# Performance work log

Measured on AMD Instinct MI355X. Metric: run time of the kernel, lower is better.

## Reference

```python
import jax, jax.numpy as jnp
import numpy as np

B, Cin, Cout, H, W = 4, 256, 256, 64, 64
DG, KH, KW = 2, 3, 3        # deformable_groups=2, kernel 3x3
K = KH * KW
CG = Cin // DG


def setup_inputs() -> dict:
    key = jax.random.key(0)
    ks = jax.random.split(key, 4)
    x = jax.random.normal(ks[0], (B, Cin, H, W), jnp.float32)
    # offset/mask-predicting 3x3 conv: 3*DG*K = 54 output channels
    # (small weights so sampled offsets stay in a realistic +-few-pixel range)
    w_off = jax.random.normal(ks[1], (3 * DG * K, Cin, KH, KW), jnp.float32) * 0.01
    b_off = jnp.zeros((3 * DG * K,), jnp.float32)
    weight = jax.random.normal(ks[2], (Cout, Cin, KH, KW), jnp.float32) * (1.0 / np.sqrt(Cin * K))
    bias = jnp.zeros((Cout,), jnp.float32)
    return {"x": x, "w_off": w_off, "b_off": b_off, "weight": weight, "bias": bias}


def _dcn_forward(x, w_off, b_off, weight, bias):
    # 1) predict offsets + modulation mask with a regular 3x3 conv
    om = jax.lax.conv_general_dilated(
        x, w_off, window_strides=(1, 1), padding=((1, 1), (1, 1)),
        dimension_numbers=('NCHW', 'OIHW', 'NCHW'))
    om = om + b_off[None, :, None, None]
    off = om[:, :2 * DG * K].reshape(B, DG, 2, K, H, W)        # [.,.,(dy,dx),k,h,w]
    mask = jax.nn.sigmoid(om[:, 2 * DG * K:]).reshape(B, DG, K, H, W)

    # 2) sampling positions: base grid (stride 1, pad 1, dilation 1) + learned offsets
    ky = jnp.repeat(jnp.arange(KH), KW).astype(jnp.float32)    # [K]
    kx = jnp.tile(jnp.arange(KW), KH).astype(jnp.float32)
    gy = jnp.arange(H, dtype=jnp.float32)
    gx = jnp.arange(W, dtype=jnp.float32)
    py = off[:, :, 0] + (gy[None, None, None, :, None] + ky[None, None, :, None, None] - 1.0)  # [B,DG,K,H,W]
    px = off[:, :, 1] + (gx[None, None, None, None, :] + kx[None, None, :, None, None] - 1.0)

    y0 = jnp.floor(py); x0 = jnp.floor(px)
    wy1 = py - y0; wx1 = px - x0
    wy0 = 1.0 - wy1; wx0 = 1.0 - wx1
    y0i = y0.astype(jnp.int32); x0i = x0.astype(jnp.int32)

    imgf = x.reshape(B, DG, CG, H * W)  # channel groups share their group's offsets

    def gather(iy, ix):
        # zero padding outside the image, as in the DCNv2 CUDA kernel
        valid = ((iy >= 0) & (iy < H) & (ix >= 0) & (ix < W)).astype(x.dtype)  # [B,DG,K,H,W]
        idx = jnp.clip(iy, 0, H - 1) * W + jnp.clip(ix, 0, W - 1)
        idx = idx.reshape(B, DG, K * H * W)
        v = jax.vmap(jax.vmap(lambda im, ii: im[:, ii]))(imgf, idx)  # [B,DG,CG,K*H*W]
        return v.reshape(B, DG, CG, K, H, W) * valid[:, :, None]

    # 3) bilinear interpolation of the 4 corners
    sampled = (gather(y0i,     x0i)     * (wy0 * wx0)[:, :, None]
             + gather(y0i,     x0i + 1) * (wy0 * wx1)[:, :, None]
             + gather(y0i + 1, x0i)     * (wy1 * wx0)[:, :, None]
             + gather(y0i + 1, x0i + 1) * (wy1 * wx1)[:, :, None])
    sampled = sampled * mask[:, :, None]  # modulation (DCNv2)

    # 4) weighted accumulation == grouped contraction over (channel, tap)
    wr = weight.reshape(Cout, DG, CG, K)
    out = jnp.einsum('odck,bdckhw->bohw', wr, sampled) + bias[None, :, None, None]
    return out


def reference(x, w_off, b_off, weight, bias):
    return _dcn_forward(x, w_off, b_off, weight, bias)
```

## Files before the change

### kernel.cpp

```cpp
#include <hip/hip_runtime.h>
#include <cstdint>

#define HW 4096

typedef __attribute__((ext_vector_type(8))) short bf16x8;
typedef __attribute__((ext_vector_type(4))) float f32x4;

__device__ __forceinline__ short f2bf(float f) {
    union { float f; uint32_t u; } v; v.f = f;
    uint32_t u = v.u;
    uint32_t r = (u + 0x7FFFu + ((u >> 16) & 1u)) >> 16;
    return (short)(r & 0xFFFFu);
}
__device__ __forceinline__ uint32_t cvtpk(float lo, float hi) {
    uint32_t r;
    asm("v_cvt_pk_bf16_f32 %0, %1, %2" : "=v"(r) : "v"(lo), "v"(hi));
    return r;
}
__device__ __forceinline__ float blo(uint32_t u) { return __uint_as_float(u << 16); }
__device__ __forceinline__ float bhi(uint32_t u) { return __uint_as_float(u & 0xFFFF0000u); }
__device__ __forceinline__ void glds16(const void* g, void* l) {
    __builtin_amdgcn_global_load_lds(
        (const __attribute__((address_space(1))) void*)g,
        (__attribute__((address_space(3))) void*)l, 16, 0, 0);
}

__global__ __launch_bounds__(256) void k_xt(
    const float* __restrict__ x, unsigned short* __restrict__ xT)
{
    __shared__ unsigned short s[64][65];
    const int t = threadIdx.x, lane = t & 63, grp = t >> 6;
    const int hw0 = blockIdx.x * 64, c0 = blockIdx.y * 64, b = blockIdx.z;
#pragma unroll
    for (int j = 0; j < 16; ++j) {
        int cc = grp * 16 + j;
        float v = x[((size_t)(b * 256 + c0 + cc)) * HW + hw0 + lane];
        s[cc][lane] = (unsigned short)f2bf(v);
    }
    __syncthreads();
#pragma unroll
    for (int j = 0; j < 16; ++j) {
        int hw2 = grp * 16 + j;
        xT[((size_t)b * HW + hw0 + hw2) * 256 + c0 + lane] = s[lane][hw2];
    }
}

__global__ __launch_bounds__(256) void k_wcvt_all(
    const float* __restrict__ weight, const float* __restrict__ w_off,
    short* __restrict__ a2r, short* __restrict__ wTb)
{
    int e = blockIdx.x * 256 + threadIdx.x;
    if (e < 589824) {
        int el = e & 7;
        int lane = (e >> 3) & 63;
        int rg = (e >> 9) & 15;
        int ss = (e >> 13) & 3;
        int j = e >> 15;
        int o = rg * 16 + (lane & 15);
        int cch = ss * 32 + (lane >> 4) * 8 + el;
        int dg = j / 9, tap = j - dg * 9;
        a2r[e] = f2bf(weight[o * 2304 + (dg * 128 + cch) * 9 + tap]);
    } else {
        int e2 = e - 589824;
        int o = e2 / 2304, r = e2 - o * 2304;
        int tap = r >> 8, c = r & 255;
        wTb[e2] = (o < 54) ? f2bf(w_off[(o * 256 + c) * 9 + tap]) : (short)0;
    }
}

__global__ __launch_bounds__(256, 4) void k_omgemm(
    const short* __restrict__ wTb, const unsigned short* __restrict__ xT,
    float* __restrict__ om2p)
{
    __shared__ short As[2][64 * 32];
    __shared__ short Bs[2][64 * 32];
    const int t = threadIdx.x;
    const int wid = __builtin_amdgcn_readfirstlane(t >> 6);
    const int lane = t & 63, quad = lane >> 4, l16 = lane & 15;
    const int n0 = blockIdx.x * 64, b = n0 >> 12;
    const int ks = blockIdx.y;
    const int nr = t >> 2;
    const int ksh = (t & 3) * 8;
    const int px = (n0 + nr) & 4095, h = px >> 6, w = px & 63;
    const unsigned short* xb = xT + (size_t)b * HW * 256;
    const int cbase = ks * 18;

    auto loadB = [&](int c) -> uint4 {
        int tap = c >> 3, c0 = (c & 7) * 32;
        int hh = h + tap / 3 - 1, ww = w + tap % 3 - 1;
        uint4 bv = {0u, 0u, 0u, 0u};
        if (hh >= 0 && hh < 64 && ww >= 0 && ww < 64)
            bv = *(const uint4*)(xb + (size_t)(hh * 64 + ww) * 256 + c0 + ksh);
        return bv;
    };

    f32x4 acc[4];
#pragma unroll
    for (int i = 0; i < 4; ++i) acc[i] = (f32x4){0.f, 0.f, 0.f, 0.f};

    uint4 bv[2];
    bv[0] = loadB(cbase);
    glds16(wTb + (size_t)nr * 2304 + cbase * 32 + ksh, &As[0][t * 8]);
    *(uint4*)&Bs[0][t * 8] = bv[0];
    bv[1] = loadB(cbase + 1);

#pragma unroll 2
    for (int i = 0; i < 18; ++i) {
        const int p = i & 1;
        __syncthreads();
        if (i < 17) {
            glds16(wTb + (size_t)nr * 2304 + (cbase + i + 1) * 32 + ksh,
                   &As[1 - p][t * 8]);
            *(uint4*)&Bs[1 - p][t * 8] = bv[(i + 1) & 1];
        }
        if (i + 2 < 18) bv[i & 1] = loadB(cbase + i + 2);
        bf16x8 bf = *(const bf16x8*)&Bs[p][(wid * 16 + l16) * 32 + quad * 8];
#pragma unroll
        for (int mi = 0; mi < 4; ++mi) {
            bf16x8 af = *(const bf16x8*)&As[p][(mi * 16 + l16) * 32 + quad * 8];
            acc[mi] = __builtin_amdgcn_mfma_f32_16x16x32_bf16(af, bf, acc[mi], 0, 0, 0);
        }
    }
    const int n = n0 + wid * 16 + l16;
#pragma unroll
    for (int mi = 0; mi < 4; ++mi)
#pragma unroll
        for (int i = 0; i < 4; ++i)
            om2p[(size_t)(ks * 64 + mi * 16 + quad * 4 + i) * 16384 + n] = acc[mi][i];
}

__global__ __launch_bounds__(256) void k_plan(
    const float* __restrict__ om2p, const float* __restrict__ b_off,
    float4* __restrict__ planw, int4* __restrict__ plani)
{
    int e = blockIdx.x * 256 + threadIdx.x;
    int n = e & 16383, s = e >> 14;
    int dg = s >= 9 ? 1 : 0, tap = s - dg * 9;
    int h = (n >> 6) & 63, w = n & 63;
    int cdy = dg * 18 + tap, cdx = cdy + 9, cms = 36 + dg * 9 + tap;
    float dy = b_off[cdy], dx = b_off[cdx], ms = b_off[cms];
#pragma unroll
    for (int cs = 0; cs < 4; ++cs) {
        const float* p = om2p + (size_t)cs * 64 * 16384;
        dy += p[(size_t)cdy * 16384 + n];
        dx += p[(size_t)cdx * 16384 + n];
        ms += p[(size_t)cms * 16384 + n];
    }
    ms = 1.f / (1.f + __expf(-ms));
    float py = dy + (float)(h + tap / 3 - 1);
    float qx = dx + (float)(w + tap % 3 - 1);
    float y0f = floorf(py), x0f = floorf(qx);
    float wy1 = py - y0f, wx1 = qx - x0f;
    float wy0 = 1.f - wy1, wx0 = 1.f - wx1;
    int y0 = (int)y0f, x0 = (int)x0f;
    int y1 = y0 + 1, x1 = x0 + 1;
    bool vy0 = (y0 >= 0) & (y0 < 64), vy1 = (y1 >= 0) & (y1 < 64);
    bool vx0 = (x0 >= 0) & (x0 < 64), vx1 = (x1 >= 0) & (x1 < 64);
    int cy0 = min(max(y0, 0), 63), cy1 = min(max(y1, 0), 63);
    int cx0 = min(max(x0, 0), 63), cx1 = min(max(x1, 0), 63);
    float4 wv;
    wv.x = (vy0 && vx0) ? wy0 * wx0 * ms : 0.f;
    wv.y = (vy0 && vx1) ? wy0 * wx1 * ms : 0.f;
    wv.z = (vy1 && vx0) ? wy1 * wx0 * ms : 0.f;
    wv.w = (vy1 && vx1) ? wy1 * wx1 * ms : 0.f;
    int4 iv = make_int4((cy0 * 64 + cx0) << 9, (cy0 * 64 + cx1) << 9,
                        (cy1 * 64 + cx0) << 9, (cy1 * 64 + cx1) << 9);
    planw[e] = wv;
    plani[e] = iv;
}

__global__ __launch_bounds__(512, 4) void k_fused(
    const short* __restrict__ A2r, const unsigned short* __restrict__ xT,
    const float4* __restrict__ planw, const int4* __restrict__ plani,
    const float* __restrict__ bias, float* __restrict__ out)
{
    __shared__ short Bs[2][4][32 * 32];
    const int t = threadIdx.x;
    const int wid = __builtin_amdgcn_readfirstlane(t >> 6);
    const int lane = t & 63;
    const int quad = lane >> 4, l16 = lane & 15;
    const int wr = wid;

    const int lin = blockIdx.x;
    const int bn = ((lin & 7) << 6) | (lin >> 3);

    const int n0 = bn * 32, b = n0 >> 12;
    const char* xbb = (const char*)xT + (size_t)b * HW * 512;
    const int px = t >> 4;
    const int cc = (t >> 2) & 3;
    const int q8 = (t & 3) * 8;
    const int n = n0 + px;

    const short* Aw = A2r + (size_t)(wr * 2) * 512 + lane * 8;

    f32x4 acc[2][2];
#pragma unroll
    for (int i = 0; i < 2; ++i)
#pragma unroll
        for (int j = 0; j < 2; ++j) acc[i][j] = (f32x4){0.f, 0.f, 0.f, 0.f};

    float4 pw[2];
    int4 pi[2];
    uint4 g[4];
    uint4 ar[8];

    auto pwload = [&](int S) { pw[S & 1] = planw[(size_t)S * 16384 + n]; };
    auto piload = [&](int S) { pi[S & 1] = plani[(size_t)S * 16384 + n]; };
    auto gather = [&](int j) {
        const int cb = ((j >= 9 ? 128 : 0) + cc * 32 + q8) * 2;
        const int4 i4 = pi[j & 1];
        g[0] = *(const uint4*)(xbb + i4.x + cb);
        g[1] = *(const uint4*)(xbb + i4.y + cb);
        g[2] = *(const uint4*)(xbb + i4.z + cb);
        g[3] = *(const uint4*)(xbb + i4.w + cb);
    };
    auto aload = [&](int j) {
#pragma unroll
        for (int ss = 0; ss < 4; ++ss)
#pragma unroll
            for (int mi = 0; mi < 2; ++mi)
                ar[ss * 2 + mi] =
                    *(const uint4*)(Aw + (size_t)(j * 4 + ss) * 8192 + mi * 512);
    };
    const int bsw = ((t & 3) ^ ((px >> 1) & 3)) * 8;
    auto packwrite = [&](int j, int buf) {
        const float4 w4 = pw[j & 1];
        float a0 = w4.x * blo(g[0].x) + w4.y * blo(g[1].x) + w4.z * blo(g[2].x) + w4.w * blo(g[3].x);
        float a1 = w4.x * bhi(g[0].x) + w4.y * bhi(g[1].x) + w4.z * bhi(g[2].x) + w4.w * bhi(g[3].x);
        float a2v = w4.x * blo(g[0].y) + w4.y * blo(g[1].y) + w4.z * blo(g[2].y) + w4.w * blo(g[3].y);
        float a3 = w4.x * bhi(g[0].y) + w4.y * bhi(g[1].y) + w4.z * bhi(g[2].y) + w4.w * bhi(g[3].y);
        float a4 = w4.x * blo(g[0].z) + w4.y * blo(g[1].z) + w4.z * blo(g[2].z) + w4.w * blo(g[3].z);
        float a5 = w4.x * bhi(g[0].z) + w4.y * bhi(g[1].z) + w4.z * bhi(g[2].z) + w4.w * bhi(g[3].z);
        float a6 = w4.x * blo(g[0].w) + w4.y * blo(g[1].w) + w4.z * blo(g[2].w) + w4.w * blo(g[3].w);
        float a7 = w4.x * bhi(g[0].w) + w4.y * bhi(g[1].w) + w4.z * bhi(g[2].w) + w4.w * bhi(g[3].w);
        uint4 o;
        o.x = cvtpk(a0, a1); o.y = cvtpk(a2v, a3);
        o.z = cvtpk(a4, a5); o.w = cvtpk(a6, a7);
        *(uint4*)&Bs[buf][cc][px * 32 + bsw] = o;
    };
    auto mfmaPhase = [&](int p) {
#pragma unroll
        for (int ss = 0; ss < 4; ++ss) {
            bf16x8 bfr[2];
#pragma unroll
            for (int ni = 0; ni < 2; ++ni) {
                const int row = ni * 16 + l16;
                bfr[ni] = *(const bf16x8*)&Bs[p][ss][row * 32 + (quad ^ ((row >> 1) & 3)) * 8];
            }
#pragma unroll
            for (int mi = 0; mi < 2; ++mi) {
                bf16x8 af = *(const bf16x8*)&ar[ss * 2 + mi];
#pragma unroll
                for (int ni = 0; ni < 2; ++ni)
                    acc[mi][ni] = __builtin_amdgcn_mfma_f32_16x16x32_bf16(
                        af, bfr[ni], acc[mi][ni], 0, 0, 0);
            }
        }
    };

    pwload(0);
    piload(0);
    gather(0);
    aload(0);
    packwrite(0, 0);
    pwload(1);
    piload(1);

#pragma unroll 2
    for (int i = 0; i < 18; ++i) {
        const int p = i & 1;
        __syncthreads();
        if (i + 1 < 18) gather(i + 1);
        if (i + 2 < 18) { pwload(i + 2); piload(i + 2); }
        __builtin_amdgcn_sched_barrier(0);
        mfmaPhase(p);
        if (i + 1 < 18) aload(i + 1);
        if (i + 1 < 18) packwrite(i + 1, 1 - p);
    }

    const int m0 = wr * 32;
#pragma unroll
    for (int mi = 0; mi < 2; ++mi)
#pragma unroll
        for (int ni = 0; ni < 2; ++ni) {
            int nn = n0 + ni * 16 + l16;
            int bidx = nn >> 12, hw = nn & 4095;
            float* op = out + (size_t)bidx * 256 * 4096 + hw;
#pragma unroll
            for (int r = 0; r < 4; ++r) {
                int m = m0 + mi * 16 + quad * 4 + r;
                op[(size_t)m * 4096] = acc[mi][ni][r] + bias[m];
            }
        }
}

extern "C" void kernel_launch(void* const* d_in, const int* in_sizes, int n_in,
                              void* d_out, int out_size, void* d_ws, size_t ws_size,
                              hipStream_t stream)
{
    const float* x      = (const float*)d_in[0];
    const float* w_off  = (const float*)d_in[1];
    const float* b_off  = (const float*)d_in[2];
    const float* weight = (const float*)d_in[3];
    const float* bias   = (const float*)d_in[4];
    float* out = (float*)d_out;
    char* ws = (char*)d_ws;

    unsigned short* xT   = (unsigned short*)(ws);
    short*          a2r  = (short*)(ws + 8388608);
    short*          wTb  = (short*)(ws + 9568256);
    float4*         planw= (float4*)(ws + 9863168);
    int4*           plani= (int4*)(ws + 14581760);
    float*          om2p = (float*)d_out;

    hipLaunchKernelGGL(k_xt, dim3(64, 4, 4), dim3(256), 0, stream, x, xT);
    hipLaunchKernelGGL(k_wcvt_all, dim3(2880), dim3(256), 0, stream,
                       weight, w_off, a2r, wTb);
    hipLaunchKernelGGL(k_omgemm, dim3(256, 4), dim3(256), 0, stream, wTb, xT, om2p);
    hipLaunchKernelGGL(k_plan, dim3(1152), dim3(256), 0, stream, om2p, b_off, planw, plani);
    hipLaunchKernelGGL(k_fused, dim3(512), dim3(512), 0, stream,
                       a2r, xT, planw, plani, bias, out);
}
```

Baseline: 142.1 us.

## Merge preprocessing kernels and fuse sampling-plan computation into main kernel

Combines the x transpose and weight conversion kernels into a single launch split by block index. It also removes the separate plan kernel: each fused block now computes bilinear weights and indices for its 32 pixels and 18 taps into shared memory, reading the partial offset sums directly. This drops two launches and the global round trip for the plan arrays. The cost is a prologue plus barrier in the main kernel and extra shared memory, which may lower occupancy. om2p now lives in the workspace instead of the output buffer.

```diff
diff --git a/kernel.cpp b/kernel.cpp
--- a/kernel.cpp
+++ b/kernel.cpp
@@ -25,46 +25,46 @@
         (__attribute__((address_space(3))) void*)l, 16, 0, 0);
 }
 
-__global__ __launch_bounds__(256) void k_xt(
-    const float* __restrict__ x, unsigned short* __restrict__ xT)
-{
-    __shared__ unsigned short s[64][65];
-    const int t = threadIdx.x, lane = t & 63, grp = t >> 6;
-    const int hw0 = blockIdx.x * 64, c0 = blockIdx.y * 64, b = blockIdx.z;
-#pragma unroll
-    for (int j = 0; j < 16; ++j) {
-        int cc = grp * 16 + j;
-        float v = x[((size_t)(b * 256 + c0 + cc)) * HW + hw0 + lane];
-        s[cc][lane] = (unsigned short)f2bf(v);
-    }
-    __syncthreads();
-#pragma unroll
-    for (int j = 0; j < 16; ++j) {
-        int hw2 = grp * 16 + j;
-        xT[((size_t)b * HW + hw0 + hw2) * 256 + c0 + lane] = s[lane][hw2];
-    }
-}
-
-__global__ __launch_bounds__(256) void k_wcvt_all(
-    const float* __restrict__ weight, const float* __restrict__ w_off,
+__global__ __launch_bounds__(256) void k_pre(
+    const float* __restrict__ x, const float* __restrict__ weight,
+    const float* __restrict__ w_off, unsigned short* __restrict__ xT,
     short* __restrict__ a2r, short* __restrict__ wTb)
 {
-    int e = blockIdx.x * 256 + threadIdx.x;
-    if (e < 589824) {
-        int el = e & 7;
-        int lane = (e >> 3) & 63;
-        int rg = (e >> 9) & 15;
-        int ss = (e >> 13) & 3;
-        int j = e >> 15;
-        int o = rg * 16 + (lane & 15);
-        int cch = ss * 32 + (lane >> 4) * 8 + el;
-        int dg = j / 9, tap = j - dg * 9;
-        a2r[e] = f2bf(weight[o * 2304 + (dg * 128 + cch) * 9 + tap]);
+    const int bid = blockIdx.x;
+    if (bid < 1024) {
+        __shared__ unsigned short s[64][65];
+        const int t = threadIdx.x, lane = t & 63, grp = t >> 6;
+        const int hw0 = (bid & 63) * 64, c0 = ((bid >> 6) & 3) * 64, b = bid >> 8;
+#pragma unroll
+        for (int j = 0; j < 16; ++j) {
+            int cc = grp * 16 + j;
+            float v = x[((size_t)(b * 256 + c0 + cc)) * HW + hw0 + lane];
+            s[cc][lane] = (unsigned short)f2bf(v);
+        }
+        __syncthreads();
+#pragma unroll
+        for (int j = 0; j < 16; ++j) {
+            int hw2 = grp * 16 + j;
+            xT[((size_t)b * HW + hw0 + hw2) * 256 + c0 + lane] = s[lane][hw2];
+        }
     } else {
-        int e2 = e - 589824;
-        int o = e2 / 2304, r = e2 - o * 2304;
-        int tap = r >> 8, c = r & 255;
-        wTb[e2] = (o < 54) ? f2bf(w_off[(o * 256 + c) * 9 + tap]) : (short)0;
+        int e = (bid - 1024) * 256 + threadIdx.x;
+        if (e < 589824) {
+            int el = e & 7;
+            int lane = (e >> 3) & 63;
+            int rg = (e >> 9) & 15;
+            int ss = (e >> 13) & 3;
+            int j = e >> 15;
+            int o = rg * 16 + (lane & 15);
+            int cch = ss * 32 + (lane >> 4) * 8 + el;
+            int dg = j / 9, tap = j - dg * 9;
+            a2r[e] = f2bf(weight[o * 2304 + (dg * 128 + cch) * 9 + tap]);
+        } else {
+            int e2 = e - 589824;
+            int o = e2 / 2304, r = e2 - o * 2304;
+            int tap = r >> 8, c = r & 255;
+            wTb[e2] = (o < 54) ? f2bf(w_off[(o * 256 + c) * 9 + tap]) : (short)0;
+        }
     }
 }
 
@@ -129,52 +129,14 @@
             om2p[(size_t)(ks * 64 + mi * 16 + quad * 4 + i) * 16384 + n] = acc[mi][i];
 }
 
-__global__ __launch_bounds__(256) void k_plan(
-    const float* __restrict__ om2p, const float* __restrict__ b_off,
-    float4* __restrict__ planw, int4* __restrict__ plani)
-{
-    int e = blockIdx.x * 256 + threadIdx.x;
-    int n = e & 16383, s = e >> 14;
-    int dg = s >= 9 ? 1 : 0, tap = s - dg * 9;
-    int h = (n >> 6) & 63, w = n & 63;
-    int cdy = dg * 18 + tap, cdx = cdy + 9, cms = 36 + dg * 9 + tap;
-    float dy = b_off[cdy], dx = b_off[cdx], ms = b_off[cms];
-#pragma unroll
-    for (int cs = 0; cs < 4; ++cs) {
-        const float* p = om2p + (size_t)cs * 64 * 16384;
-        dy += p[(size_t)cdy * 16384 + n];
-        dx += p[(size_t)cdx * 16384 + n];
-        ms += p[(size_t)cms * 16384 + n];
-    }
-    ms = 1.f / (1.f + __expf(-ms));
-    float py = dy + (float)(h + tap / 3 - 1);
-    float qx = dx + (float)(w + tap % 3 - 1);
-    float y0f = floorf(py), x0f = floorf(qx);
-    float wy1 = py - y0f, wx1 = qx - x0f;
-    float wy0 = 1.f - wy1, wx0 = 1.f - wx1;
-    int y0 = (int)y0f, x0 = (int)x0f;
-    int y1 = y0 + 1, x1 = x0 + 1;
-    bool vy0 = (y0 >= 0) & (y0 < 64), vy1 = (y1 >= 0) & (y1 < 64);
-    bool vx0 = (x0 >= 0) & (x0 < 64), vx1 = (x1 >= 0) & (x1 < 64);
-    int cy0 = min(max(y0, 0), 63), cy1 = min(max(y1, 0), 63);
-    int cx0 = min(max(x0, 0), 63), cx1 = min(max(x1, 0), 63);
-    float4 wv;
-    wv.x = (vy0 && vx0) ? wy0 * wx0 * ms : 0.f;
-    wv.y = (vy0 && vx1) ? wy0 * wx1 * ms : 0.f;
-    wv.z = (vy1 && vx0) ? wy1 * wx0 * ms : 0.f;
-    wv.w = (vy1 && vx1) ? wy1 * wx1 * ms : 0.f;
-    int4 iv = make_int4((cy0 * 64 + cx0) << 9, (cy0 * 64 + cx1) << 9,
-                        (cy1 * 64 + cx0) << 9, (cy1 * 64 + cx1) << 9);
-    planw[e] = wv;
-    plani[e] = iv;
-}
-
 __global__ __launch_bounds__(512, 4) void k_fused(
     const short* __restrict__ A2r, const unsigned short* __restrict__ xT,
-    const float4* __restrict__ planw, const int4* __restrict__ plani,
+    const float* __restrict__ om2p, const float* __restrict__ b_off,
     const float* __restrict__ bias, float* __restrict__ out)
 {
     __shared__ short Bs[2][4][32 * 32];
+    __shared__ float4 PlnW[18][32];
+    __shared__ int4   PlnI[18][32];
     const int t = threadIdx.x;
     const int wid = __builtin_amdgcn_readfirstlane(t >> 6);
     const int lane = t & 63;
@@ -189,7 +151,45 @@
     const int px = t >> 4;
     const int cc = (t >> 2) & 3;
     const int q8 = (t & 3) * 8;
-    const int n = n0 + px;
+
+    for (int s = wid; s < 18; s += 8) {
+        if (lane < 32) {
+            const int nn = n0 + lane;
+            const int dg = s >= 9 ? 1 : 0, tap = s - dg * 9;
+            const int hh = (nn >> 6) & 63, ww2 = nn & 63;
+            const int cdy = dg * 18 + tap, cdx = cdy + 9, cms = 36 + dg * 9 + tap;
+            float dy = b_off[cdy], dx = b_off[cdx], ms = b_off[cms];
+#pragma unroll
+            for (int cs2 = 0; cs2 < 4; ++cs2) {
+                const float* pp = om2p + (size_t)cs2 * 64 * 16384;
+                dy += pp[(size_t)cdy * 16384 + nn];
+                dx += pp[(size_t)cdx * 16384 + nn];
+                ms += pp[(size_t)cms * 16384 + nn];
+            }
+            ms = 1.f / (1.f + __expf(-ms));
+            float py = dy + (float)(hh + tap / 3 - 1);
+            float qx = dx + (float)(ww2 + tap % 3 - 1);
+            float y0f = floorf(py), x0f = floorf(qx);
+            float wy1 = py - y0f, wx1 = qx - x0f;
+            float wy0 = 1.f - wy1, wx0 = 1.f - wx1;
+            int y0 = (int)y0f, x0 = (int)x0f;
+            int y1 = y0 + 1, x1 = x0 + 1;
+            bool vy0 = (y0 >= 0) & (y0 < 64), vy1 = (y1 >= 0) & (y1 < 64);
+            bool vx0 = (x0 >= 0) & (x0 < 64), vx1 = (x1 >= 0) & (x1 < 64);
+            int cy0 = min(max(y0, 0), 63), cy1 = min(max(y1, 0), 63);
+            int cx0 = min(max(x0, 0), 63), cx1 = min(max(x1, 0), 63);
+            float4 wv;
+            wv.x = (vy0 && vx0) ? wy0 * wx0 * ms : 0.f;
+            wv.y = (vy0 && vx1) ? wy0 * wx1 * ms : 0.f;
+            wv.z = (vy1 && vx0) ? wy1 * wx0 * ms : 0.f;
+            wv.w = (vy1 && vx1) ? wy1 * wx1 * ms : 0.f;
+            int4 iv = make_int4((cy0 * 64 + cx0) << 9, (cy0 * 64 + cx1) << 9,
+                                (cy1 * 64 + cx0) << 9, (cy1 * 64 + cx1) << 9);
+            PlnW[s][lane] = wv;
+            PlnI[s][lane] = iv;
+        }
+    }
+    __syncthreads();
 
     const short* Aw = A2r + (size_t)(wr * 2) * 512 + lane * 8;
 
@@ -204,8 +204,8 @@
     uint4 g[4];
     uint4 ar[8];
 
-    auto pwload = [&](int S) { pw[S & 1] = planw[(size_t)S * 16384 + n]; };
-    auto piload = [&](int S) { pi[S & 1] = plani[(size_t)S * 16384 + n]; };
+    auto pwload = [&](int S) { pw[S & 1] = PlnW[S][px]; };
+    auto piload = [&](int S) { pi[S & 1] = PlnI[S][px]; };
     auto gather = [&](int j) {
         const int cb = ((j >= 9 ? 128 : 0) + cc * 32 + q8) * 2;
         const int4 i4 = pi[j & 1];
@@ -309,15 +309,11 @@
     unsigned short* xT   = (unsigned short*)(ws);
     short*          a2r  = (short*)(ws + 8388608);
     short*          wTb  = (short*)(ws + 9568256);
-    float4*         planw= (float4*)(ws + 9863168);
-    int4*           plani= (int4*)(ws + 14581760);
-    float*          om2p = (float*)d_out;
-
-    hipLaunchKernelGGL(k_xt, dim3(64, 4, 4), dim3(256), 0, stream, x, xT);
-    hipLaunchKernelGGL(k_wcvt_all, dim3(2880), dim3(256), 0, stream,
-                       weight, w_off, a2r, wTb);
+    float*          om2p = (float*)(ws + 9863168);
+
+    hipLaunchKernelGGL(k_pre, dim3(3904), dim3(256), 0, stream,
+                       x, weight, w_off, xT, a2r, wTb);
     hipLaunchKernelGGL(k_omgemm, dim3(256, 4), dim3(256), 0, stream, wTb, xT, om2p);
-    hipLaunchKernelGGL(k_plan, dim3(1152), dim3(256), 0, stream, om2p, b_off, planw, plani);
     hipLaunchKernelGGL(k_fused, dim3(512), dim3(512), 0, stream,
-                       a2r, xT, planw, plani, bias, out);
-}
+                       a2r, xT, om2p, b_off, bias, out);
+}
```

New measurement: 129.2 us. 1.1x faster.
